# Optimization experiments

Measured on AMD Instinct MI355X. Metric: run time of the kernel, lower is better.

Reference implementation:

```python
import jax, jax.numpy as jnp
import numpy as np

CLAMP = 60.0
EPS = 1e-4

def _make_weights(N, alpha_logits, delta_logits, beta_logits):
    alpha = jax.nn.sigmoid(alpha_logits)   # [C,H]
    delta = jax.nn.sigmoid(delta_logits)
    beta = jax.nn.sigmoid(beta_logits)
    A = alpha * beta                        # [C,H]
    r = jnp.clip(1.0 - alpha * delta, EPS, 1.0 - EPS)
    t = jnp.arange(N, dtype=jnp.float32)[:, None, None]   # [N,1,1]
    logr = jnp.clip(jnp.log(r) * t, -CLAMP, CLAMP)        # [N,C,H]
    return A, jnp.exp(logr), jnp.exp(-logr)

def _ema_fwd(x, A, eta, r_pos, r_neg):
    # x: [B,N,C] -> y: [B,N,C]
    z = A * x[..., None] * r_neg            # [B,N,C,H]
    h = jnp.cumsum(z, axis=1) * r_pos       # [B,N,C,H]
    return jnp.sum(eta * h, axis=-1)        # [B,N,C]

def reference(x, alpha_logits, delta_logits, beta_logits, eta, proj_w, proj_b):
    B, N, C = x.shape
    A, r_pos, r_neg = _make_weights(N, alpha_logits, delta_logits, beta_logits)
    xf = x.astype(jnp.float32)
    y_fwd = _ema_fwd(xf, A, eta, r_pos, r_neg)
    y_bwd = _ema_fwd(xf[:, ::-1], A, eta, r_pos, r_neg)[:, ::-1]
    z = jnp.concatenate([y_fwd, y_bwd], axis=-1).astype(x.dtype)  # [B,N,2C]
    return z @ proj_w.T + proj_b            # [B,N,C]

def setup_inputs():
    key = jax.random.key(0)
    ks = jax.random.split(key, 7)
    B, N, C, H = 8, 4096, 512, 4
    return {
        "x": jax.random.normal(ks[0], (B, N, C), dtype=jnp.float32),
        "alpha_logits": jax.random.normal(ks[1], (C, H), dtype=jnp.float32),
        "delta_logits": jax.random.normal(ks[2], (C, H), dtype=jnp.float32),
        "beta_logits": jax.random.normal(ks[3], (C, H), dtype=jnp.float32),
        "eta": jax.random.normal(ks[4], (C, H), dtype=jnp.float32) * 0.02,
        "proj_w": jax.random.normal(ks[5], (C, 2 * C), dtype=jnp.float32) / np.sqrt(2.0 * C),
        "proj_b": jax.random.normal(ks[6], (C,), dtype=jnp.float32) * 0.01,
    }
```

## Files before the change

kernel.cpp:

```cpp
#include <hip/hip_runtime.h>
#include <hip/hip_bf16.h>

#define B_ 8
#define N_ 4096
#define C_ 512
#define H_ 4
#define EPS_ 1e-4f
#define E60P 1.14200739e26f
#define E60M 8.7565108e-27f

typedef __attribute__((ext_vector_type(8))) short short8;
typedef __attribute__((ext_vector_type(4))) float floatx4;
typedef __attribute__((ext_vector_type(2))) float floatx2;
typedef __attribute__((ext_vector_type(4))) unsigned short ushort4_t;
typedef unsigned short ushort_t;

__device__ __forceinline__ float sigmoidf_(float v) {
    return 1.0f / (1.0f + expf(-v));
}

__device__ __forceinline__ int pk_off(int t, int w, int k0, int ks, int f,
                                      int lane8, int kb) {
    return ((((t * 2 + w) * 16 + k0) * 2 + ks) * 4 + f) * 512 + lane8 * 8 + kb;
}

__device__ __forceinline__ void gload16(const void* g, void* l) {
    __builtin_amdgcn_global_load_lds(
        (const __attribute__((address_space(1))) void*)g,
        (__attribute__((address_space(3))) void*)l, 16, 0, 0);
}

__global__ __launch_bounds__(256, 8) void k_partials5(
    const float* __restrict__ x, const float* __restrict__ al,
    const float* __restrict__ dl, const float* __restrict__ bl,
    float* __restrict__ P)
{
    int bid   = blockIdx.x;
    int chunk = bid & 15;
    int ct    = (bid >> 4) & 7;
    int b     = (bid >> 7) & 7;
    int dir   = bid >> 10;
    int lane  = threadIdx.x & 63;
    int wave  = threadIdx.x >> 6;
    int c     = ct * 64 + lane;
    int sub   = chunk * 4 + wave;
    int t0f   = sub * 64;
    int t0b   = (63 - sub) * 64;

    float aa[4], dd[4], bb[4];
    { float4 v = ((const float4*)al)[c]; aa[0]=v.x; aa[1]=v.y; aa[2]=v.z; aa[3]=v.w; }
    { float4 v = ((const float4*)dl)[c]; dd[0]=v.x; dd[1]=v.y; dd[2]=v.z; dd[3]=v.w; }
    { float4 v = ((const float4*)bl)[c]; bb[0]=v.x; bb[1]=v.y; bb[2]=v.z; bb[3]=v.w; }

    float A[H_], ri[H_], Lh[H_];
    #pragma unroll
    for (int h = 0; h < H_; ++h) {
        float alpha = sigmoidf_(aa[h]);
        float delta = sigmoidf_(dd[h]);
        float beta  = sigmoidf_(bb[h]);
        A[h] = alpha * beta;
        float r = fminf(fmaxf(1.0f - alpha * delta, EPS_), 1.0f - EPS_);
        Lh[h] = logf(r);
        ri[h] = 1.0f / r;
    }
    floatx2 ri2[2]  = {{ri[0], ri[1]}, {ri[2], ri[3]}};
    floatx2 AEP2[2] = {{A[0] * E60P, A[1] * E60P}, {A[2] * E60P, A[3] * E60P}};

    const float* xp = x + ((size_t)b * N_ + t0f) * C_ + c;

    int   t0   = dir ? t0b : t0f;
    floatx2 Ae2[2], T2[2];
    #pragma unroll
    for (int p = 0; p < 2; ++p) {
        Ae2[p] = (floatx2){A[2*p]   * expf(fminf(-Lh[2*p]   * (float)t0, 60.0f)),
                           A[2*p+1] * expf(fminf(-Lh[2*p+1] * (float)t0, 60.0f))};
        T2[p]  = (floatx2){0.f, 0.f};
    }

    if (dir == 0) {
        float cur[8];
        #pragma unroll
        for (int j = 0; j < 8; ++j) cur[j] = xp[(size_t)j * C_];
        #pragma unroll 1
        for (int g = 0; g < 8; ++g) {
            float nxt[8];
            if (g < 7) {
                #pragma unroll
                for (int j = 0; j < 8; ++j)
                    nxt[j] = xp[(size_t)(g * 8 + 8 + j) * C_];
            }
            #pragma unroll
            for (int j = 0; j < 8; ++j) {
                floatx2 xv2 = {cur[j], cur[j]};
                #pragma unroll
                for (int p = 0; p < 2; ++p) {
                    T2[p] += Ae2[p] * xv2;
                    Ae2[p] = __builtin_elementwise_min(Ae2[p] * ri2[p], AEP2[p]);
                }
            }
            if (g < 7) {
                #pragma unroll
                for (int j = 0; j < 8; ++j) cur[j] = nxt[j];
            }
        }
        float* pp = P + ((size_t)b * 64 + sub) * (H_ * C_) + c;
        pp[0]      = T2[0].x;  pp[C_]     = T2[0].y;
        pp[2 * C_] = T2[1].x;  pp[3 * C_] = T2[1].y;
    } else {
        float cur[8];
        #pragma unroll
        for (int j = 0; j < 8; ++j) cur[j] = xp[(size_t)(63 - j) * C_];
        #pragma unroll 1
        for (int g = 0; g < 8; ++g) {
            float nxt[8];
            if (g < 7) {
                #pragma unroll
                for (int j = 0; j < 8; ++j)
                    nxt[j] = xp[(size_t)(63 - (g * 8 + 8 + j)) * C_];
            }
            #pragma unroll
            for (int j = 0; j < 8; ++j) {
                floatx2 xv2 = {cur[j], cur[j]};
                #pragma unroll
                for (int p = 0; p < 2; ++p) {
                    T2[p] += Ae2[p] * xv2;
                    Ae2[p] = __builtin_elementwise_min(Ae2[p] * ri2[p], AEP2[p]);
                }
            }
            if (g < 7) {
                #pragma unroll
                for (int j = 0; j < 8; ++j) cur[j] = nxt[j];
            }
        }
        float* pp = P + ((size_t)(8 + b) * 64 + (63 - sub)) * (H_ * C_) + c;
        pp[0]      = T2[0].x;  pp[C_]     = T2[0].y;
        pp[2 * C_] = T2[1].x;  pp[3 * C_] = T2[1].y;
    }
}

__global__ __launch_bounds__(256) void k_scan(float* __restrict__ P)
{
    int bid = blockIdx.x;
    int ct  = bid & 7;
    int b   = (bid >> 3) & 7;
    int dir = bid >> 6;
    int cl  = threadIdx.x & 63;
    int h   = threadIdx.x >> 6;
    int c   = ct * 64 + cl;

    float* base = P + ((size_t)(dir * 8 + b) * 64) * (H_ * C_) + h * C_ + c;

    float v[64];
    #pragma unroll
    for (int s = 0; s < 64; ++s) v[s] = base[s * (H_ * C_)];

    float run = 0.0f;
    #pragma unroll
    for (int s = 0; s < 64; ++s) { float t = v[s]; v[s] = run; run += t; }

    #pragma unroll
    for (int s = 0; s < 64; ++s) base[s * (H_ * C_)] = v[s];
}

__global__ __launch_bounds__(256, 8) void k_apply5(
    const float* __restrict__ x, const float* __restrict__ al,
    const float* __restrict__ dl, const float* __restrict__ bl,
    const float* __restrict__ eta, const float* __restrict__ P,
    ushort_t* __restrict__ Zp)
{
    int bid   = blockIdx.x;
    int chunk = bid & 15;
    int ct    = (bid >> 4) & 7;
    int b     = (bid >> 7) & 7;
    int dir   = bid >> 10;
    int lane  = threadIdx.x & 63;
    int wave  = threadIdx.x >> 6;
    int c     = ct * 64 + lane;
    int sub   = chunk * 4 + wave;
    int t0f   = sub * 64;
    int t0b   = (63 - sub) * 64;

    int ksv = lane >> 5, qv = (lane >> 3) & 3, kbv = lane & 7;
    int mt  = b * 32 + (t0f >> 7);
    int wq  = (t0f >> 6) & 1;

    float aa[4], dd[4], bb[4], ee[4];
    { float4 v = ((const float4*)al )[c]; aa[0]=v.x; aa[1]=v.y; aa[2]=v.z; aa[3]=v.w; }
    { float4 v = ((const float4*)dl )[c]; dd[0]=v.x; dd[1]=v.y; dd[2]=v.z; dd[3]=v.w; }
    { float4 v = ((const float4*)bl )[c]; bb[0]=v.x; bb[1]=v.y; bb[2]=v.z; bb[3]=v.w; }
    { float4 v = ((const float4*)eta)[c]; ee[0]=v.x; ee[1]=v.y; ee[2]=v.z; ee[3]=v.w; }

    float A[H_], rr[H_], ri[H_], Lh[H_];
    #pragma unroll
    for (int h = 0; h < H_; ++h) {
        float alpha = sigmoidf_(aa[h]);
        float delta = sigmoidf_(dd[h]);
        float beta  = sigmoidf_(bb[h]);
        A[h] = alpha * beta;
        float r = fminf(fmaxf(1.0f - alpha * delta, EPS_), 1.0f - EPS_);
        Lh[h] = logf(r);
        rr[h] = r;
        ri[h] = 1.0f / r;
    }
    const floatx2 E2M = {E60M, E60M};
    floatx2 ri2[2]  = {{ri[0], ri[1]}, {ri[2], ri[3]}};
    floatx2 rr2[2]  = {{rr[0], rr[1]}, {rr[2], rr[3]}};
    floatx2 ee2[2]  = {{ee[0], ee[1]}, {ee[2], ee[3]}};
    floatx2 AEP2[2] = {{A[0] * E60P, A[1] * E60P}, {A[2] * E60P, A[3] * E60P}};

    const float* xp = x + ((size_t)b * N_ + t0f) * C_ + c;

    if (dir == 0) {
        int offcF = pk_off(mt, wq, ct, ksv, 0, qv * 16, kbv);
        const float* cp = P + ((size_t)b * 64 + sub) * (H_ * C_) + c;
        floatx2 Ae2[2], em2[2], S2[2];
        #pragma unroll
        for (int p = 0; p < 2; ++p) {
            Ae2[p] = (floatx2){A[2*p]   * expf(fminf(-Lh[2*p]   * (float)t0f, 60.0f)),
                               A[2*p+1] * expf(fminf(-Lh[2*p+1] * (float)t0f, 60.0f))};
            em2[p] = (floatx2){expf(fmaxf( Lh[2*p]   * (float)t0f, -60.0f)),
                               expf(fmaxf( Lh[2*p+1] * (float)t0f, -60.0f))};
            S2[p]  = (floatx2){cp[(2*p) * C_], cp[(2*p+1) * C_]};
        }
        float cur[8];
        #pragma unroll
        for (int j = 0; j < 8; ++j) cur[j] = xp[(size_t)j * C_];
        #pragma unroll 1
        for (int g = 0; g < 8; ++g) {
            float nxt[8];
            if (g < 7) {
                #pragma unroll
                for (int j = 0; j < 8; ++j)
                    nxt[j] = xp[(size_t)(g * 8 + 8 + j) * C_];
            }
            #pragma unroll
            for (int j = 0; j < 8; ++j) {
                int i = g * 8 + j;
                floatx2 xv2 = {cur[j], cur[j]};
                floatx2 acc = {0.f, 0.f};
                #pragma unroll
                for (int p = 0; p < 2; ++p) {
                    S2[p] += Ae2[p] * xv2;
                    Ae2[p] = __builtin_elementwise_min(Ae2[p] * ri2[p], AEP2[p]);
                    acc   += ee2[p] * (em2[p] * S2[p]);
                    em2[p] = __builtin_elementwise_max(em2[p] * rr2[p], E2M);
                }
                float y = acc.x + acc.y;
                __hip_bfloat16 yb = __float2bfloat16(y);
                Zp[offcF + (i >> 4) * 512 + (i & 15) * 8] = *(ushort_t*)&yb;
            }
            if (g < 7) {
                #pragma unroll
                for (int j = 0; j < 8; ++j) cur[j] = nxt[j];
            }
        }
    } else {
        int offcB = pk_off(mt, wq, 8 + ct, ksv, 0, qv * 16, kbv);
        const float* cp = P + ((size_t)(8 + b) * 64 + (63 - sub)) * (H_ * C_) + c;
        floatx2 Ae2[2], em2[2], S2[2];
        #pragma unroll
        for (int p = 0; p < 2; ++p) {
            Ae2[p] = (floatx2){A[2*p]   * expf(fminf(-Lh[2*p]   * (float)t0b, 60.0f)),
                               A[2*p+1] * expf(fminf(-Lh[2*p+1] * (float)t0b, 60.0f))};
            em2[p] = (floatx2){expf(fmaxf( Lh[2*p]   * (float)t0b, -60.0f)),
                               expf(fmaxf( Lh[2*p+1] * (float)t0b, -60.0f))};
            S2[p]  = (floatx2){cp[(2*p) * C_], cp[(2*p+1) * C_]};
        }
        float cur[8];
        #pragma unroll
        for (int j = 0; j < 8; ++j) cur[j] = xp[(size_t)(63 - j) * C_];
        #pragma unroll 1
        for (int g = 0; g < 8; ++g) {
            float nxt[8];
            if (g < 7) {
                #pragma unroll
                for (int j = 0; j < 8; ++j)
                    nxt[j] = xp[(size_t)(63 - (g * 8 + 8 + j)) * C_];
            }
            #pragma unroll
            for (int j = 0; j < 8; ++j) {
                int i = 63 - (g * 8 + j);
                floatx2 xv2 = {cur[j], cur[j]};
                floatx2 acc = {0.f, 0.f};
                #pragma unroll
                for (int p = 0; p < 2; ++p) {
                    S2[p] += Ae2[p] * xv2;
                    Ae2[p] = __builtin_elementwise_min(Ae2[p] * ri2[p], AEP2[p]);
                    acc   += ee2[p] * (em2[p] * S2[p]);
                    em2[p] = __builtin_elementwise_max(em2[p] * rr2[p], E2M);
                }
                float y = acc.x + acc.y;
                __hip_bfloat16 yb = __float2bfloat16(y);
                Zp[offcB + (i >> 4) * 512 + (i & 15) * 8] = *(ushort_t*)&yb;
            }
            if (g < 7) {
                #pragma unroll
                for (int j = 0; j < 8; ++j) cur[j] = nxt[j];
            }
        }
    }
}

__global__ __launch_bounds__(256) void k_cvtw2(const float* __restrict__ w,
                                               ushort_t* __restrict__ Wp)
{
    int i4 = blockIdx.x * 256 + threadIdx.x;
    int i  = i4 << 2;
    int n = i >> 10, k = i & 1023;
    int nt = n >> 7, rn = n & 127;
    int k0 = k >> 6, kk = k & 63;
    int off = pk_off(nt, rn >> 6, k0, kk >> 5, (rn >> 4) & 3,
                     ((kk >> 3) & 3) * 16 + (rn & 15), kk & 7);
    float4 v = ((const float4*)w)[i4];
    ushort4_t r;
    { __hip_bfloat16 t = __float2bfloat16(v.x); r.x = *(ushort_t*)&t; }
    { __hip_bfloat16 t = __float2bfloat16(v.y); r.y = *(ushort_t*)&t; }
    { __hip_bfloat16 t = __float2bfloat16(v.z); r.z = *(ushort_t*)&t; }
    { __hip_bfloat16 t = __float2bfloat16(v.w); r.w = *(ushort_t*)&t; }
    *(ushort4_t*)&Wp[off] = r;
}

__global__ __launch_bounds__(256, 4) void k_gemm3(
    const ushort_t* __restrict__ Zp, const ushort_t* __restrict__ Wp,
    const float* __restrict__ bias, float* __restrict__ out)
{
    __shared__ __align__(16) char lds[32768];
    char*  ldsA = lds;
    char*  ldsB = lds + 16384;
    float* stg  = (float*)lds;

    int tid  = threadIdx.x;
    int lane = tid & 63, wave = tid >> 6;
    int wm   = wave & 1, wn = wave >> 1;
    int fr   = lane & 15, quad = lane >> 4;

    int bid = blockIdx.x;
    int mt  = ((bid >> 5) << 3) | (bid & 7);
    int nt  = (bid >> 3) & 3;
    int m0  = mt * 128, n0 = nt * 128;

    const ushort_t* Az = Zp + ((size_t)(mt * 2) * 16) * 4096;
    const ushort_t* Bz = Wp + ((size_t)(nt * 2) * 16) * 4096;

    floatx4 acc[4][4];
    #pragma unroll
    for (int mf = 0; mf < 4; ++mf)
        #pragma unroll
        for (int nf = 0; nf < 4; ++nf)
            acc[mf][nf] = (floatx4){0.f, 0.f, 0.f, 0.f};

    for (int k0 = 0; k0 < 16; ++k0) {
        const ushort_t* As = Az + (size_t)k0 * 4096;
        const ushort_t* Bs = Bz + (size_t)k0 * 4096;
        #pragma unroll
        for (int w = 0; w < 2; ++w)
            #pragma unroll
            for (int inst = 0; inst < 2; ++inst) {
                gload16(As + w * 65536 + inst * 2048 + tid * 8,
                        ldsA + w * 8192 + inst * 4096 + tid * 16);
                gload16(Bs + w * 65536 + inst * 2048 + tid * 8,
                        ldsB + w * 8192 + inst * 4096 + tid * 16);
            }
        asm volatile("s_waitcnt vmcnt(0)" ::: "memory");
        __syncthreads();

        #pragma unroll
        for (int ks = 0; ks < 2; ++ks) {
            short8 af[4], bf[4];
            #pragma unroll
            for (int f = 0; f < 4; ++f) {
                af[f] = *(const short8*)(ldsA + wm * 8192 + (ks * 4 + f) * 1024 + lane * 16);
                bf[f] = *(const short8*)(ldsB + wn * 8192 + (ks * 4 + f) * 1024 + lane * 16);
            }
            #pragma unroll
            for (int mf = 0; mf < 4; ++mf)
                #pragma unroll
                for (int nf = 0; nf < 4; ++nf)
                    acc[mf][nf] = __builtin_amdgcn_mfma_f32_16x16x32_bf16(
                        af[mf], bf[nf], acc[mf][nf], 0, 0, 0);
        }
        __syncthreads();
    }

    int rrow = tid >> 3;
    int seg  = tid & 7;
    int gcol = n0 + seg * 16;

    #pragma unroll
    for (int ch = 0; ch < 4; ++ch) {
        if ((wave & 1) == (ch >> 1)) {
            int ml = (ch & 1) * 2;
            #pragma unroll
            for (int mi = 0; mi < 2; ++mi) {
                #pragma unroll
                for (int nf = 0; nf < 4; ++nf) {
                    int col = wn * 64 + nf * 16 + fr;
                    #pragma unroll
                    for (int rg = 0; rg < 4; ++rg) {
                        int row = mi * 16 + quad * 4 + rg;
                        stg[row * 132 + col] = acc[ml + mi][nf][rg];
                    }
                }
            }
        }
        __syncthreads();
        {
            int gm = m0 + ch * 32 + rrow;
            const float* s = &stg[rrow * 132 + seg * 16];
            #pragma unroll
            for (int k = 0; k < 4; ++k) {
                float4 v  = *(const float4*)&s[k * 4];
                float4 bv = *(const float4*)&bias[gcol + k * 4];
                v.x += bv.x; v.y += bv.y; v.z += bv.z; v.w += bv.w;
                *(float4*)&out[(size_t)gm * 512 + gcol + k * 4] = v;
            }
        }
        __syncthreads();
    }
}

extern "C" void kernel_launch(void* const* d_in, const int* in_sizes, int n_in,
                              void* d_out, int out_size, void* d_ws, size_t ws_size,
                              hipStream_t stream)
{
    const float* x  = (const float*)d_in[0];
    const float* al = (const float*)d_in[1];
    const float* dl = (const float*)d_in[2];
    const float* bl = (const float*)d_in[3];
    const float* et = (const float*)d_in[4];
    const float* pw = (const float*)d_in[5];
    const float* pb = (const float*)d_in[6];
    float* out = (float*)d_out;

    ushort_t* Zp = (ushort_t*)d_ws;
    float*    P  = (float*)((char*)d_ws + 67108864);
    ushort_t* Wp = (ushort_t*)((char*)d_ws + 75497472);

    hipLaunchKernelGGL(k_cvtw2,     dim3(512),  dim3(256), 0, stream, pw, Wp);
    hipLaunchKernelGGL(k_partials5, dim3(2048), dim3(256), 0, stream, x, al, dl, bl, P);
    hipLaunchKernelGGL(k_scan,      dim3(128),  dim3(256), 0, stream, P);
    hipLaunchKernelGGL(k_apply5,    dim3(2048), dim3(256), 0, stream, x, al, dl, bl, et, P, Zp);
    hipLaunchKernelGGL(k_gemm3,     dim3(1024), dim3(256), 0, stream, Zp, Wp, pb, out);
}
```

Measured before the change: 220.6 us.

## Fuse EMA partials, scan and apply into one kernel with LDS chunk scan

```diff
diff --git a/kernel.cpp b/kernel.cpp
--- a/kernel.cpp
+++ b/kernel.cpp
@@ -30,159 +30,41 @@
         (__attribute__((address_space(3))) void*)l, 16, 0, 0);
 }
 
-__global__ __launch_bounds__(256, 8) void k_partials5(
+__global__ __launch_bounds__(1024, 4) void k_ema_fused(
     const float* __restrict__ x, const float* __restrict__ al,
     const float* __restrict__ dl, const float* __restrict__ bl,
-    float* __restrict__ P)
-{
-    int bid   = blockIdx.x;
-    int chunk = bid & 15;
-    int ct    = (bid >> 4) & 7;
-    int b     = (bid >> 7) & 7;
-    int dir   = bid >> 10;
-    int lane  = threadIdx.x & 63;
-    int wave  = threadIdx.x >> 6;
-    int c     = ct * 64 + lane;
-    int sub   = chunk * 4 + wave;
-    int t0f   = sub * 64;
-    int t0b   = (63 - sub) * 64;
-
-    float aa[4], dd[4], bb[4];
-    { float4 v = ((const float4*)al)[c]; aa[0]=v.x; aa[1]=v.y; aa[2]=v.z; aa[3]=v.w; }
-    { float4 v = ((const float4*)dl)[c]; dd[0]=v.x; dd[1]=v.y; dd[2]=v.z; dd[3]=v.w; }
-    { float4 v = ((const float4*)bl)[c]; bb[0]=v.x; bb[1]=v.y; bb[2]=v.z; bb[3]=v.w; }
-
-    float A[H_], ri[H_], Lh[H_];
-    #pragma unroll
-    for (int h = 0; h < H_; ++h) {
-        float alpha = sigmoidf_(aa[h]);
-        float delta = sigmoidf_(dd[h]);
-        float beta  = sigmoidf_(bb[h]);
-        A[h] = alpha * beta;
-        float r = fminf(fmaxf(1.0f - alpha * delta, EPS_), 1.0f - EPS_);
-        Lh[h] = logf(r);
-        ri[h] = 1.0f / r;
-    }
-    floatx2 ri2[2]  = {{ri[0], ri[1]}, {ri[2], ri[3]}};
-    floatx2 AEP2[2] = {{A[0] * E60P, A[1] * E60P}, {A[2] * E60P, A[3] * E60P}};
-
-    const float* xp = x + ((size_t)b * N_ + t0f) * C_ + c;
-
-    int   t0   = dir ? t0b : t0f;
-    floatx2 Ae2[2], T2[2];
-    #pragma unroll
-    for (int p = 0; p < 2; ++p) {
-        Ae2[p] = (floatx2){A[2*p]   * expf(fminf(-Lh[2*p]   * (float)t0, 60.0f)),
-                           A[2*p+1] * expf(fminf(-Lh[2*p+1] * (float)t0, 60.0f))};
-        T2[p]  = (floatx2){0.f, 0.f};
-    }
-
-    if (dir == 0) {
-        float cur[8];
-        #pragma unroll
-        for (int j = 0; j < 8; ++j) cur[j] = xp[(size_t)j * C_];
-        #pragma unroll 1
-        for (int g = 0; g < 8; ++g) {
-            float nxt[8];
-            if (g < 7) {
-                #pragma unroll
-                for (int j = 0; j < 8; ++j)
-                    nxt[j] = xp[(size_t)(g * 8 + 8 + j) * C_];
-            }
-            #pragma unroll
-            for (int j = 0; j < 8; ++j) {
-                floatx2 xv2 = {cur[j], cur[j]};
-                #pragma unroll
-                for (int p = 0; p < 2; ++p) {
-                    T2[p] += Ae2[p] * xv2;
-                    Ae2[p] = __builtin_elementwise_min(Ae2[p] * ri2[p], AEP2[p]);
-                }
-            }
-            if (g < 7) {
-                #pragma unroll
-                for (int j = 0; j < 8; ++j) cur[j] = nxt[j];
-            }
-        }
-        float* pp = P + ((size_t)b * 64 + sub) * (H_ * C_) + c;
-        pp[0]      = T2[0].x;  pp[C_]     = T2[0].y;
-        pp[2 * C_] = T2[1].x;  pp[3 * C_] = T2[1].y;
-    } else {
-        float cur[8];
-        #pragma unroll
-        for (int j = 0; j < 8; ++j) cur[j] = xp[(size_t)(63 - j) * C_];
-        #pragma unroll 1
-        for (int g = 0; g < 8; ++g) {
-            float nxt[8];
-            if (g < 7) {
-                #pragma unroll
-                for (int j = 0; j < 8; ++j)
-                    nxt[j] = xp[(size_t)(63 - (g * 8 + 8 + j)) * C_];
-            }
-            #pragma unroll
-            for (int j = 0; j < 8; ++j) {
-                floatx2 xv2 = {cur[j], cur[j]};
-                #pragma unroll
-                for (int p = 0; p < 2; ++p) {
-                    T2[p] += Ae2[p] * xv2;
-                    Ae2[p] = __builtin_elementwise_min(Ae2[p] * ri2[p], AEP2[p]);
-                }
-            }
-            if (g < 7) {
-                #pragma unroll
-                for (int j = 0; j < 8; ++j) cur[j] = nxt[j];
-            }
-        }
-        float* pp = P + ((size_t)(8 + b) * 64 + (63 - sub)) * (H_ * C_) + c;
-        pp[0]      = T2[0].x;  pp[C_]     = T2[0].y;
-        pp[2 * C_] = T2[1].x;  pp[3 * C_] = T2[1].y;
-    }
-}
-
-__global__ __launch_bounds__(256) void k_scan(float* __restrict__ P)
+    const float* __restrict__ eta, const float* __restrict__ pw,
+    ushort_t* __restrict__ Zp, ushort_t* __restrict__ Wp)
 {
     int bid = blockIdx.x;
-    int ct  = bid & 7;
-    int b   = (bid >> 3) & 7;
-    int dir = bid >> 6;
-    int cl  = threadIdx.x & 63;
-    int h   = threadIdx.x >> 6;
-    int c   = ct * 64 + cl;
-
-    float* base = P + ((size_t)(dir * 8 + b) * 64) * (H_ * C_) + h * C_ + c;
-
-    float v[64];
-    #pragma unroll
-    for (int s = 0; s < 64; ++s) v[s] = base[s * (H_ * C_)];
-
-    float run = 0.0f;
-    #pragma unroll
-    for (int s = 0; s < 64; ++s) { float t = v[s]; v[s] = run; run += t; }
-
-    #pragma unroll
-    for (int s = 0; s < 64; ++s) base[s * (H_ * C_)] = v[s];
-}
-
-__global__ __launch_bounds__(256, 8) void k_apply5(
-    const float* __restrict__ x, const float* __restrict__ al,
-    const float* __restrict__ dl, const float* __restrict__ bl,
-    const float* __restrict__ eta, const float* __restrict__ P,
-    ushort_t* __restrict__ Zp)
-{
-    int bid   = blockIdx.x;
-    int chunk = bid & 15;
-    int ct    = (bid >> 4) & 7;
-    int b     = (bid >> 7) & 7;
-    int dir   = bid >> 10;
-    int lane  = threadIdx.x & 63;
-    int wave  = threadIdx.x >> 6;
-    int c     = ct * 64 + lane;
-    int sub   = chunk * 4 + wave;
-    int t0f   = sub * 64;
-    int t0b   = (63 - sub) * 64;
-
-    int ksv = lane >> 5, qv = (lane >> 3) & 3, kbv = lane & 7;
-    int mt  = b * 32 + (t0f >> 7);
-    int wq  = (t0f >> 6) & 1;
+    int tid = threadIdx.x;
+
+    if (bid >= 256) {
+        int i4 = (bid - 256) * 1024 + tid;
+        int i  = i4 << 2;
+        int n = i >> 10, k = i & 1023;
+        int nt = n >> 7, rn = n & 127;
+        int k0 = k >> 6, kk = k & 63;
+        int off = pk_off(nt, rn >> 6, k0, kk >> 5, (rn >> 4) & 3,
+                         ((kk >> 3) & 3) * 16 + (rn & 15), kk & 7);
+        float4 v = ((const float4*)pw)[i4];
+        ushort4_t r;
+        { __hip_bfloat16 t = __float2bfloat16(v.x); r.x = *(ushort_t*)&t; }
+        { __hip_bfloat16 t = __float2bfloat16(v.y); r.y = *(ushort_t*)&t; }
+        { __hip_bfloat16 t = __float2bfloat16(v.z); r.z = *(ushort_t*)&t; }
+        { __hip_bfloat16 t = __float2bfloat16(v.w); r.w = *(ushort_t*)&t; }
+        *(ushort4_t*)&Wp[off] = r;
+        return;
+    }
+
+    __shared__ float slds[32][128];
+
+    int dir  = bid & 1;
+    int b    = (bid >> 1) & 7;
+    int ct16 = bid >> 4;
+    int c5   = tid & 31;
+    int sg   = tid >> 5;
+    int c    = ct16 * 32 + c5;
 
     float aa[4], dd[4], bb[4], ee[4];
     { float4 v = ((const float4*)al )[c]; aa[0]=v.x; aa[1]=v.y; aa[2]=v.z; aa[3]=v.w; }
@@ -208,34 +90,96 @@
     floatx2 ee2[2]  = {{ee[0], ee[1]}, {ee[2], ee[3]}};
     floatx2 AEP2[2] = {{A[0] * E60P, A[1] * E60P}, {A[2] * E60P, A[3] * E60P}};
 
-    const float* xp = x + ((size_t)b * N_ + t0f) * C_ + c;
-
-    if (dir == 0) {
-        int offcF = pk_off(mt, wq, ct, ksv, 0, qv * 16, kbv);
-        const float* cp = P + ((size_t)b * 64 + sub) * (H_ * C_) + c;
-        floatx2 Ae2[2], em2[2], S2[2];
-        #pragma unroll
-        for (int p = 0; p < 2; ++p) {
-            Ae2[p] = (floatx2){A[2*p]   * expf(fminf(-Lh[2*p]   * (float)t0f, 60.0f)),
-                               A[2*p+1] * expf(fminf(-Lh[2*p+1] * (float)t0f, 60.0f))};
-            em2[p] = (floatx2){expf(fmaxf( Lh[2*p]   * (float)t0f, -60.0f)),
-                               expf(fmaxf( Lh[2*p+1] * (float)t0f, -60.0f))};
-            S2[p]  = (floatx2){cp[(2*p) * C_], cp[(2*p+1) * C_]};
-        }
+    int  t0 = sg * 128;
+    int  r0 = dir ? (N_ - 1 - t0) : t0;
+    long sC = dir ? -(long)C_ : (long)C_;
+    const float* xb = x + ((size_t)b * N_ + r0) * C_ + c;
+
+    floatx2 Ae2[2], T2[2];
+    #pragma unroll
+    for (int p = 0; p < 2; ++p) {
+        Ae2[p] = (floatx2){A[2*p]   * expf(fminf(-Lh[2*p]   * (float)t0, 60.0f)),
+                           A[2*p+1] * expf(fminf(-Lh[2*p+1] * (float)t0, 60.0f))};
+        T2[p]  = (floatx2){0.f, 0.f};
+    }
+    {
         float cur[8];
         #pragma unroll
-        for (int j = 0; j < 8; ++j) cur[j] = xp[(size_t)j * C_];
+        for (int j = 0; j < 8; ++j) cur[j] = xb[(long)j * sC];
         #pragma unroll 1
-        for (int g = 0; g < 8; ++g) {
+        for (int g = 0; g < 16; ++g) {
             float nxt[8];
-            if (g < 7) {
+            if (g < 15) {
                 #pragma unroll
                 for (int j = 0; j < 8; ++j)
-                    nxt[j] = xp[(size_t)(g * 8 + 8 + j) * C_];
+                    nxt[j] = xb[(long)(g * 8 + 8 + j) * sC];
             }
             #pragma unroll
             for (int j = 0; j < 8; ++j) {
-                int i = g * 8 + j;
+                floatx2 xv2 = {cur[j], cur[j]};
+                #pragma unroll
+                for (int p = 0; p < 2; ++p) {
+                    T2[p] += Ae2[p] * xv2;
+                    Ae2[p] = __builtin_elementwise_min(Ae2[p] * ri2[p], AEP2[p]);
+                }
+            }
+            if (g < 15) {
+                #pragma unroll
+                for (int j = 0; j < 8; ++j) cur[j] = nxt[j];
+            }
+        }
+    }
+    *(float4*)&slds[sg][c5 * 4] = (float4){T2[0].x, T2[0].y, T2[1].x, T2[1].y};
+
+    __syncthreads();
+
+    if (tid < 128) {
+        float run = 0.f;
+        #pragma unroll
+        for (int s = 0; s < 32; ++s) {
+            float v = slds[s][tid];
+            slds[s][tid] = run;
+            run += v;
+        }
+    }
+    __syncthreads();
+
+    floatx2 em2[2], S2[2];
+    {
+        float4 pf = *(const float4*)&slds[sg][c5 * 4];
+        S2[0] = (floatx2){pf.x, pf.y};
+        S2[1] = (floatx2){pf.z, pf.w};
+    }
+    #pragma unroll
+    for (int p = 0; p < 2; ++p) {
+        Ae2[p] = (floatx2){A[2*p]   * expf(fminf(-Lh[2*p]   * (float)t0, 60.0f)),
+                           A[2*p+1] * expf(fminf(-Lh[2*p+1] * (float)t0, 60.0f))};
+        em2[p] = (floatx2){expf(fmaxf( Lh[2*p]   * (float)t0, -60.0f)),
+                           expf(fmaxf( Lh[2*p+1] * (float)t0, -60.0f))};
+    }
+
+    int cl  = (ct16 & 1) * 32 + c5;
+    int k0c = (dir ? 8 : 0) + (ct16 >> 1);
+    int mtv = b * 32 + (dir ? (31 - sg) : sg);
+    int ksv = cl >> 5, qv = (cl >> 3) & 3, kbv = cl & 7;
+    int offc0 = pk_off(mtv, 0, k0c, ksv, 0, qv * 16, kbv);
+    int offc1 = pk_off(mtv, 1, k0c, ksv, 0, qv * 16, kbv);
+
+    {
+        float cur[8];
+        #pragma unroll
+        for (int j = 0; j < 8; ++j) cur[j] = xb[(long)j * sC];
+        #pragma unroll 1
+        for (int g = 0; g < 16; ++g) {
+            float nxt[8];
+            if (g < 15) {
+                #pragma unroll
+                for (int j = 0; j < 8; ++j)
+                    nxt[j] = xb[(long)(g * 8 + 8 + j) * sC];
+            }
+            #pragma unroll
+            for (int j = 0; j < 8; ++j) {
+                int jj = g * 8 + j;
                 floatx2 xv2 = {cur[j], cur[j]};
                 floatx2 acc = {0.f, 0.f};
                 #pragma unroll
@@ -247,77 +191,18 @@
                 }
                 float y = acc.x + acc.y;
                 __hip_bfloat16 yb = __float2bfloat16(y);
-                Zp[offcF + (i >> 4) * 512 + (i & 15) * 8] = *(ushort_t*)&yb;
-            }
-            if (g < 7) {
+                int q6 = (jj >> 6) & 1;
+                int wq = dir ? (1 - q6) : q6;
+                int ii = dir ? (63 - (jj & 63)) : (jj & 63);
+                int off = (wq ? offc1 : offc0) + ((ii >> 4) << 9) + ((ii & 15) << 3);
+                Zp[off] = *(ushort_t*)&yb;
+            }
+            if (g < 15) {
                 #pragma unroll
                 for (int j = 0; j < 8; ++j) cur[j] = nxt[j];
             }
         }
-    } else {
-        int offcB = pk_off(mt, wq, 8 + ct, ksv, 0, qv * 16, kbv);
-        const float* cp = P + ((size_t)(8 + b) * 64 + (63 - sub)) * (H_ * C_) + c;
-        floatx2 Ae2[2], em2[2], S2[2];
-        #pragma unroll
-        for (int p = 0; p < 2; ++p) {
-            Ae2[p] = (floatx2){A[2*p]   * expf(fminf(-Lh[2*p]   * (float)t0b, 60.0f)),
-                               A[2*p+1] * expf(fminf(-Lh[2*p+1] * (float)t0b, 60.0f))};
-            em2[p] = (floatx2){expf(fmaxf( Lh[2*p]   * (float)t0b, -60.0f)),
-                               expf(fmaxf( Lh[2*p+1] * (float)t0b, -60.0f))};
-            S2[p]  = (floatx2){cp[(2*p) * C_], cp[(2*p+1) * C_]};
-        }
-        float cur[8];
-        #pragma unroll
-        for (int j = 0; j < 8; ++j) cur[j] = xp[(size_t)(63 - j) * C_];
-        #pragma unroll 1
-        for (int g = 0; g < 8; ++g) {
-            float nxt[8];
-            if (g < 7) {
-                #pragma unroll
-                for (int j = 0; j < 8; ++j)
-                    nxt[j] = xp[(size_t)(63 - (g * 8 + 8 + j)) * C_];
-            }
-            #pragma unroll
-            for (int j = 0; j < 8; ++j) {
-                int i = 63 - (g * 8 + j);
-                floatx2 xv2 = {cur[j], cur[j]};
-                floatx2 acc = {0.f, 0.f};
-                #pragma unroll
-                for (int p = 0; p < 2; ++p) {
-                    S2[p] += Ae2[p] * xv2;
-                    Ae2[p] = __builtin_elementwise_min(Ae2[p] * ri2[p], AEP2[p]);
-                    acc   += ee2[p] * (em2[p] * S2[p]);
-                    em2[p] = __builtin_elementwise_max(em2[p] * rr2[p], E2M);
-                }
-                float y = acc.x + acc.y;
-                __hip_bfloat16 yb = __float2bfloat16(y);
-                Zp[offcB + (i >> 4) * 512 + (i & 15) * 8] = *(ushort_t*)&yb;
-            }
-            if (g < 7) {
-                #pragma unroll
-                for (int j = 0; j < 8; ++j) cur[j] = nxt[j];
-            }
-        }
-    }
-}
-
-__global__ __launch_bounds__(256) void k_cvtw2(const float* __restrict__ w,
-                                               ushort_t* __restrict__ Wp)
-{
-    int i4 = blockIdx.x * 256 + threadIdx.x;
-    int i  = i4 << 2;
-    int n = i >> 10, k = i & 1023;
-    int nt = n >> 7, rn = n & 127;
-    int k0 = k >> 6, kk = k & 63;
-    int off = pk_off(nt, rn >> 6, k0, kk >> 5, (rn >> 4) & 3,
-                     ((kk >> 3) & 3) * 16 + (rn & 15), kk & 7);
-    float4 v = ((const float4*)w)[i4];
-    ushort4_t r;
-    { __hip_bfloat16 t = __float2bfloat16(v.x); r.x = *(ushort_t*)&t; }
-    { __hip_bfloat16 t = __float2bfloat16(v.y); r.y = *(ushort_t*)&t; }
-    { __hip_bfloat16 t = __float2bfloat16(v.z); r.z = *(ushort_t*)&t; }
-    { __hip_bfloat16 t = __float2bfloat16(v.w); r.w = *(ushort_t*)&t; }
-    *(ushort4_t*)&Wp[off] = r;
+    }
 }
 
 __global__ __launch_bounds__(256, 4) void k_gemm3(
@@ -433,12 +318,10 @@
     float* out = (float*)d_out;
 
     ushort_t* Zp = (ushort_t*)d_ws;
-    float*    P  = (float*)((char*)d_ws + 67108864);
-    ushort_t* Wp = (ushort_t*)((char*)d_ws + 75497472);
-
-    hipLaunchKernelGGL(k_cvtw2,     dim3(512),  dim3(256), 0, stream, pw, Wp);
-    hipLaunchKernelGGL(k_partials5, dim3(2048), dim3(256), 0, stream, x, al, dl, bl, P);
-    hipLaunchKernelGGL(k_scan,      dim3(128),  dim3(256), 0, stream, P);
-    hipLaunchKernelGGL(k_apply5,    dim3(2048), dim3(256), 0, stream, x, al, dl, bl, et, P, Zp);
-    hipLaunchKernelGGL(k_gemm3,     dim3(1024), dim3(256), 0, stream, Zp, Wp, pb, out);
-}
+    ushort_t* Wp = (ushort_t*)((char*)d_ws + 67108864);
+
+    hipLaunchKernelGGL(k_ema_fused, dim3(384),  dim3(1024), 0, stream,
+                       x, al, dl, bl, et, pw, Zp, Wp);
+    hipLaunchKernelGGL(k_gemm3,     dim3(1024), dim3(256),  0, stream,
+                       Zp, Wp, pb, out);
+}
```

Measured after the change: 202.8 us. 1.09x faster.
